# Performance work log

Measured on AMD Instinct MI355X. Metric: run time of the kernel, lower is better.

Reference implementation:

```python
import jax, jax.numpy as jnp
import numpy as np

N_HEADS = 16
DIM = 1024
BS, SLEN = 2, 2048
EPS = 1e-12  # F.normalize eps


def setup_inputs() -> dict:
    key = jax.random.key(0)
    ks = jax.random.split(key, 10)
    d = DIM
    inp = {
        "x": jax.random.normal(ks[0], (BS, SLEN, d), dtype=jnp.float32),
        # causal attention mask, as produced by get_masks(causal=True)
        "mask": jnp.tril(jnp.ones((SLEN, SLEN), dtype=bool))[None].repeat(BS, axis=0),
        "Wq": jax.random.normal(ks[1], (d, d), dtype=jnp.float32) / np.sqrt(d),
        "bq": jax.random.normal(ks[2], (d,), dtype=jnp.float32) * 0.02,
        "Wk": jax.random.normal(ks[3], (d, d), dtype=jnp.float32) / np.sqrt(d),
        "bk": jax.random.normal(ks[4], (d,), dtype=jnp.float32) * 0.02,
        "Wv": jax.random.normal(ks[5], (d, d), dtype=jnp.float32) / np.sqrt(d),
        "bv": jax.random.normal(ks[6], (d,), dtype=jnp.float32) * 0.02,
        "Wo": jax.random.normal(ks[7], (d, d), dtype=jnp.float32) / np.sqrt(d),
        "bo": jax.random.normal(ks[8], (d,), dtype=jnp.float32) * 0.02,
        # learnable scale for normalized (cosine) attention
        "attention_scale": jnp.ones((1,), dtype=jnp.float32) / np.sqrt(d // N_HEADS),
    }
    return inp


def _shape(t, bs, h, dph):
    # (bs, len, dim) -> (bs, h, len, dph)
    return t.reshape(bs, -1, h, dph).transpose(0, 2, 1, 3)


def reference(x, mask, Wq, bq, Wk, bk, Wv, bv, Wo, bo, attention_scale):
    bs, qlen, dim = x.shape
    h = N_HEADS
    dph = dim // h

    q = _shape(x @ Wq + bq, bs, h, dph)  # (bs, h, qlen, dph)
    k = _shape(x @ Wk + bk, bs, h, dph)
    v = _shape(x @ Wv + bv, bs, h, dph)

    # normalized (cosine) attention: L2-normalize q and k, learned scale
    q = q / jnp.maximum(jnp.linalg.norm(q, axis=-1, keepdims=True), EPS)
    k = k / jnp.maximum(jnp.linalg.norm(k, axis=-1, keepdims=True), EPS)
    q = q * attention_scale

    scores = jnp.einsum("bhqd,bhkd->bhqk", q, k)  # (bs, h, qlen, klen)
    scores = jnp.where(mask[:, None, :, :], scores, -jnp.inf)
    weights = jax.nn.softmax(scores, axis=-1)

    ctx = jnp.einsum("bhqk,bhkd->bhqd", weights, v)
    ctx = ctx.transpose(0, 2, 1, 3).reshape(bs, qlen, dim)
    return ctx @ Wo + bo
```

## Files before the change

kernel.cpp:

```cpp
#include <hip/hip_runtime.h>
#include <math.h>

#define NH 16
#define DPH 64
#define SLEN 2048
#define BSZ 2
#define DIM 1024
#define NTOK (BSZ * SLEN)
#define LOG2E 1.44269504088896f

typedef unsigned short ushortT;
typedef __attribute__((ext_vector_type(8))) short short8;
typedef __attribute__((ext_vector_type(4))) short s16x4;
typedef __attribute__((ext_vector_type(4))) float f32x4;

typedef __attribute__((address_space(1))) const unsigned int gu32c;
typedef __attribute__((address_space(3))) unsigned int lu32;

__device__ __forceinline__ void gld16(const void* g, void* l) {
    __builtin_amdgcn_global_load_lds((gu32c*)g, (lu32*)l, 16, 0, 0);
}

__device__ __forceinline__ ushortT f2bf(float f) {
    unsigned int u = __builtin_bit_cast(unsigned int, f);
    u = u + 0x7fffu + ((u >> 16) & 1u);
    return (ushortT)(u >> 16);
}

__global__ __launch_bounds__(256) void cvt_x(const float* __restrict__ x,
                                             ushortT* __restrict__ xb) {
    size_t i = (size_t)blockIdx.x * 256 + threadIdx.x;
    float4 a = *(const float4*)&x[i * 8];
    float4 b = *(const float4*)&x[i * 8 + 4];
    short8 v;
    v[0] = (short)f2bf(a.x); v[1] = (short)f2bf(a.y);
    v[2] = (short)f2bf(a.z); v[3] = (short)f2bf(a.w);
    v[4] = (short)f2bf(b.x); v[5] = (short)f2bf(b.y);
    v[6] = (short)f2bf(b.z); v[7] = (short)f2bf(b.w);
    *(short8*)&xb[i * 8] = v;
}

__global__ __launch_bounds__(256) void cvt_wt(const float* __restrict__ W0, const float* __restrict__ W1,
                                              const float* __restrict__ W2, const float* __restrict__ W3,
                                              ushortT* __restrict__ T0, ushortT* __restrict__ T1,
                                              ushortT* __restrict__ T2, ushortT* __restrict__ T3) {
    const float* W = blockIdx.z == 0 ? W0 : blockIdx.z == 1 ? W1 : blockIdx.z == 2 ? W2 : W3;
    ushortT* T = blockIdx.z == 0 ? T0 : blockIdx.z == 1 ? T1 : blockIdx.z == 2 ? T2 : T3;
    __shared__ float tile[64][65];
    const int tid = threadIdx.x;
    const int kb = blockIdx.y * 64, nb = blockIdx.x * 64;
#pragma unroll
    for (int it = 0; it < 4; it++) {
        int chunk = it * 256 + tid;
        int r = chunk >> 4, c4 = (chunk & 15) * 4;
        *(float4*)&tile[r][c4] = *(const float4*)&W[(size_t)(kb + r) * DIM + nb + c4];
    }
    __syncthreads();
#pragma unroll
    for (int it = 0; it < 2; it++) {
        int chunk = it * 256 + tid;
        int n = chunk >> 3, k8 = (chunk & 7) * 8;
        short8 o;
#pragma unroll
        for (int j = 0; j < 8; j++) o[j] = (short)f2bf(tile[k8 + j][n]);
        *(short8*)&T[(size_t)(nb + n) * DIM + kb + k8] = o;
    }
}

__global__ __launch_bounds__(512, 2) void gemm_qkv8(const ushortT* __restrict__ A,
                                                    const ushortT* __restrict__ Bt,
                                                    const float* __restrict__ bq,
                                                    const float* __restrict__ bk,
                                                    const float* __restrict__ bv,
                                                    const float* __restrict__ ascale,
                                                    ushortT* __restrict__ Qb,
                                                    ushortT* __restrict__ Kb,
                                                    ushortT* __restrict__ VF) {
    __shared__ __align__(16) ushortT lds[65536];
    const int tid = threadIdx.x;
    const int lane = tid & 63, wid = tid >> 6;
    const int wm = wid >> 2, wn = wid & 3;
    const int lo = lane & 15, hi = lane >> 4;
    const int bid = blockIdx.x;
    const int swz = (bid & 7) * 24 + (bid >> 3);
    const int bx = swz % 12, by = swz / 12;
    const int row0 = by * 256, col0 = bx * 256;
    const int srow2 = tid >> 2, sc = tid & 3;
    f32x4 acc[8][4] = {};
    short8 af[4], bfr[4];

    auto stage = [&](int isA, int buf, int ksh, int kt) {
        const ushortT* g = isA ? A : Bt;
        int r0 = isA ? row0 : col0;
        int base = (isA ? 0 : 32768) + (buf * 2 + ksh) * 8192;
#pragma unroll
        for (int r = 0; r < 2; r++) {
            int rl = r * 128 + srow2;
            int gch = sc ^ ((rl >> 1) & 3);
            gld16(&g[(size_t)(r0 + rl) * DIM + kt * 64 + ksh * 32 + gch * 8],
                  &lds[base + r * 4096 + tid * 8]);
        }
    };
    auto loadA = [&](int buf, int ks, int mh) {
        int base = (buf * 2 + ks) * 8192;
#pragma unroll
        for (int mm = 0; mm < 4; mm++) {
            int row = wm * 128 + (mh * 4 + mm) * 16 + lo;
            af[mm] = *(const short8*)&lds[base + row * 32 + (hi ^ ((row >> 1) & 3)) * 8];
        }
    };
    auto loadB = [&](int buf, int ks) {
        int base = 32768 + (buf * 2 + ks) * 8192;
#pragma unroll
        for (int n = 0; n < 4; n++) {
            int row = wn * 64 + n * 16 + lo;
            bfr[n] = *(const short8*)&lds[base + row * 32 + (hi ^ ((row >> 1) & 3)) * 8];
        }
    };
    auto mfma16 = [&](int mh) {
        __builtin_amdgcn_s_setprio(1);
#pragma unroll
        for (int mm = 0; mm < 4; mm++)
#pragma unroll
            for (int n = 0; n < 4; n++)
                acc[mh * 4 + mm][n] = __builtin_amdgcn_mfma_f32_16x16x32_bf16(
                    af[mm], bfr[n], acc[mh * 4 + mm][n], 0, 0, 0);
        __builtin_amdgcn_s_setprio(0);
    };

    stage(1, 0, 0, 0); stage(0, 0, 0, 0);
    stage(1, 0, 1, 0); stage(0, 0, 1, 0);
    stage(1, 1, 0, 1); stage(0, 1, 0, 1);

#pragma unroll 1
    for (int it = 0; it < 8; ++it) {
        const int o = it * 2 + 1;
        const bool more = (it < 7);
        asm volatile("s_waitcnt vmcnt(8)" ::: "memory");
        asm volatile("s_barrier" ::: "memory");
        loadA(0, 0, 0); loadB(0, 0);
        stage(1, 1, 1, o);
        mfma16(0);
        asm volatile("s_barrier" ::: "memory");
        loadA(0, 0, 1);
        stage(0, 1, 1, o);
        mfma16(1);
        asm volatile("s_waitcnt vmcnt(8)" ::: "memory");
        asm volatile("s_barrier" ::: "memory");
        loadA(0, 1, 0); loadB(0, 1);
        if (more) stage(1, 0, 0, o + 1);
        mfma16(0);
        asm volatile("s_barrier" ::: "memory");
        loadA(0, 1, 1);
        if (more) stage(0, 0, 0, o + 1);
        mfma16(1);
        if (more) { asm volatile("s_waitcnt vmcnt(8)" ::: "memory"); }
        else      { asm volatile("s_waitcnt vmcnt(4)" ::: "memory"); }
        asm volatile("s_barrier" ::: "memory");
        loadA(1, 0, 0); loadB(1, 0);
        if (more) stage(1, 0, 1, o + 1);
        mfma16(0);
        asm volatile("s_barrier" ::: "memory");
        loadA(1, 0, 1);
        if (more) stage(0, 0, 1, o + 1);
        mfma16(1);
        if (more) { asm volatile("s_waitcnt vmcnt(8)" ::: "memory"); }
        else      { asm volatile("s_waitcnt vmcnt(0)" ::: "memory"); }
        asm volatile("s_barrier" ::: "memory");
        loadA(1, 1, 0); loadB(1, 1);
        if (more) stage(1, 1, 0, o + 2);
        mfma16(0);
        asm volatile("s_barrier" ::: "memory");
        loadA(1, 1, 1);
        if (more) stage(0, 1, 0, o + 2);
        mfma16(1);
    }
    __syncthreads();

    const int cg = col0 + wn * 64;
    const int which = cg >> 10;
    const int cwin = cg & 1023;
    const int h = cwin >> 6;
    const int t0g = row0 + wm * 128;
    const int b = t0g >> 11, tok0 = t0g & (SLEN - 1);
    const float* bias = which == 0 ? bq : which == 1 ? bk : bv;

    float bb4[4];
#pragma unroll
    for (int n = 0; n < 4; n++) bb4[n] = bias[cwin + n * 16 + lo];
#pragma unroll
    for (int m = 0; m < 8; m++)
#pragma unroll
        for (int n = 0; n < 4; n++)
#pragma unroll
            for (int r = 0; r < 4; r++) acc[m][n][r] += bb4[n];

    if (which < 2) {
        float asc = (which == 0) ? ascale[0] * LOG2E : 1.0f;
#pragma unroll
        for (int m = 0; m < 8; m++)
#pragma unroll
            for (int r = 0; r < 4; r++) {
                float ss = acc[m][0][r] * acc[m][0][r] + acc[m][1][r] * acc[m][1][r] +
                           acc[m][2][r] * acc[m][2][r] + acc[m][3][r] * acc[m][3][r];
#pragma unroll
                for (int o = 8; o > 0; o >>= 1) ss += __shfl_xor(ss, o);
                float sc2 = asc / fmaxf(sqrtf(ss), 1e-12f);
#pragma unroll
                for (int n = 0; n < 4; n++) acc[m][n][r] *= sc2;
            }
    }

    ushortT* tl = &lds[wid * 8192];
    if (which < 2) {
#pragma unroll
        for (int m = 0; m < 8; m++)
#pragma unroll
            for (int n = 0; n < 4; n++)
#pragma unroll
                for (int r = 0; r < 4; r++) {
                    int row = m * 16 + 4 * hi + r;
                    int c = n * 2 + (lo >> 3);
                    tl[row * 64 + ((c ^ (row & 7)) << 3) + (lo & 7)] = f2bf(acc[m][n][r]);
                }
        ushortT* op = which == 0 ? Qb : Kb;
        const size_t base = ((size_t)(b * NH + h) * SLEN + tok0) * DPH;
#pragma unroll
        for (int j = 0; j < 16; j++) {
            int cid = j * 64 + lane;
            int rowL = cid >> 3, c = cid & 7;
            uint4 v = *(const uint4*)&tl[rowL * 64 + ((c ^ (rowL & 7)) << 3)];
            *(uint4*)&op[base + (size_t)cid * 8] = v;
        }
    } else {
#pragma unroll
        for (int m = 0; m < 8; m++)
#pragma unroll
            for (int n = 0; n < 4; n++)
#pragma unroll
                for (int r = 0; r < 4; r++) {
                    int row = m * 16 + 4 * hi + r;
                    int c = n * 2 + (lo >> 3);
                    tl[row * 64 + ((c ^ ((row >> 3) & 7)) << 3) + (lo & 7)] = f2bf(acc[m][n][r]);
                }
        const int bh = b * NH + h;
        const int kt0 = tok0 >> 6;
#pragma unroll
        for (int i = 0; i < 16; i++) {
            int kk = i >> 3;
            int c = i & 7;
            int jd = c >> 1, ks2 = c & 1;
            int colL = jd * 16 + lo;
            int c2 = colL >> 3;
            short8 v;
#pragma unroll
            for (int e = 0; e < 8; e++) {
                int rowL = kk * 64 + ks2 * 32 + 8 * hi + e;
                v[e] = (short)tl[rowL * 64 + ((c2 ^ ((rowL >> 3) & 7)) << 3) + (colL & 7)];
            }
            *(short8*)&VF[((size_t)bh * 32 + kt0 + kk) * 4096 + (size_t)(c * 64 + lane) * 8] = v;
        }
    }
}

__global__ __launch_bounds__(256) void gemm_oproj(const ushortT* __restrict__ A,
                                                  const ushortT* __restrict__ Bt,
                                                  const float* __restrict__ bias,
                                                  float* __restrict__ outF) {
    __shared__ __align__(16) unsigned char lbuf[32768];
    ushortT* As = (ushortT*)lbuf;
    ushortT* Bs = (ushortT*)(lbuf + 8192);
    const int tid = threadIdx.x;
    const int lane = tid & 63, wid = tid >> 6;
    const int wr = wid >> 1, wc = wid & 1;
    const int lo = lane & 15, hi = lane >> 4;
    const int row0 = blockIdx.y * 64, col0 = blockIdx.x * 128;
    const int r8 = lane >> 3, sp = lane & 7;
    const int srcoff = (sp ^ r8) << 3;
    f32x4 acc[2][4] = {};

    for (int kc = 0; kc < DIM; kc += 64) {
        __syncthreads();
#pragma unroll
        for (int it = 0; it < 2; it++) {
            int seg = it * 4 + wid;
            int row = seg * 8 + r8;
            gld16(&A[(size_t)(row0 + row) * DIM + kc + srcoff], &As[seg * 512]);
        }
#pragma unroll
        for (int it = 0; it < 4; it++) {
            int seg = it * 4 + wid;
            int row = seg * 8 + r8;
            gld16(&Bt[(size_t)(col0 + row) * DIM + kc + srcoff], &Bs[seg * 512]);
        }
        __syncthreads();
#pragma unroll
        for (int ks = 0; ks < 2; ks++) {
            short8 af[2], bfr[4];
#pragma unroll
            for (int m = 0; m < 2; m++) {
                int row = wr * 32 + m * 16 + lo;
                af[m] = *(const short8*)&As[row * 64 + (((ks * 4 + hi) ^ (row & 7)) << 3)];
            }
#pragma unroll
            for (int n = 0; n < 4; n++) {
                int row = wc * 64 + n * 16 + lo;
                bfr[n] = *(const short8*)&Bs[row * 64 + (((ks * 4 + hi) ^ (row & 7)) << 3)];
            }
#pragma unroll
            for (int m = 0; m < 2; m++)
#pragma unroll
                for (int n = 0; n < 4; n++)
                    acc[m][n] = __builtin_amdgcn_mfma_f32_16x16x32_bf16(af[m], bfr[n], acc[m][n], 0, 0, 0);
        }
    }

    float bb[4];
#pragma unroll
    for (int n = 0; n < 4; n++) bb[n] = bias[col0 + wc * 64 + n * 16 + lo];
#pragma unroll
    for (int m = 0; m < 2; m++)
#pragma unroll
        for (int n = 0; n < 4; n++)
#pragma unroll
            for (int r = 0; r < 4; r++) acc[m][n][r] += bb[n];

    __syncthreads();
    float* tl = (float*)(lbuf + wid * 8192);
#pragma unroll
    for (int m = 0; m < 2; m++)
#pragma unroll
        for (int n = 0; n < 4; n++)
#pragma unroll
            for (int r = 0; r < 4; r++) {
                int row = m * 16 + hi * 4 + r;
                int col = n * 16 + lo;
                int cc = col >> 2;
                tl[row * 64 + ((cc ^ (row & 7)) << 2) + (col & 3)] = acc[m][n][r];
            }
#pragma unroll
    for (int j = 0; j < 8; j++) {
        int cid = j * 64 + lane;
        int rowR = cid >> 4, cc = cid & 15;
        f32x4 v = *(const f32x4*)&tl[rowR * 64 + ((cc ^ (rowR & 7)) << 2)];
        int rg = row0 + wr * 32 + rowR;
        int cgl = col0 + wc * 64 + cc * 4;
        *(f32x4*)&outF[(size_t)rg * DIM + cgl] = v;
    }
}

__global__ __launch_bounds__(512, 4) void attn(const ushortT* __restrict__ Q,
                                               const ushortT* __restrict__ K,
                                               const ushortT* __restrict__ VF,
                                               const float* __restrict__ scale,
                                               ushortT* __restrict__ ctx) {
    __shared__ __align__(16) ushortT Ks[64 * 64];
    __shared__ __align__(16) ushortT Ps[8 * 16 * 64];
    const int tid = threadIdx.x, lane = tid & 63, wid = tid >> 6;
    const int wg = wid & 3, sg = wid >> 2;
    const int bh = blockIdx.x, p = blockIdx.y;
    const int qt = sg ? p : 31 - p;
    const int kbmax = 31 - p;
    const size_t hb = (size_t)bh * SLEN * DPH;
    const int lo = lane & 15, hi = lane >> 4;
    const float mshift = fabsf(scale[0]) * LOG2E;

    short8 aq[2];
    {
        const int qrow = qt * 64 + wg * 16 + lo;
#pragma unroll
        for (int ks = 0; ks < 2; ks++)
            aq[ks] = *(const short8*)&Q[hb + (size_t)qrow * DPH + ks * 32 + 8 * hi];
    }

    const int srow = tid >> 3, sslot = tid & 7;
    const int sldsoff = srow * 64 + ((sslot ^ (srow & 7)) << 3);
    uint4 kr = *(const uint4*)&K[hb + (size_t)srow * DPH + sslot * 8];
    *(uint4*)&Ks[sldsoff] = kr;
    __syncthreads();

    f32x4 accd[4] = {};
    float lp = 0.f;

    for (int kb = 0; kb <= kbmax; kb++) {
        if (kb < kbmax)
            kr = *(const uint4*)&K[hb + (size_t)((kb + 1) * 64 + srow) * DPH + sslot * 8];

        if (kb <= qt) {
            short8 bv[8];
            const ushortT* vt = &VF[(((size_t)bh * 32 + kb) * 512 + lane) * 8];
#pragma unroll
            for (int c = 0; c < 8; c++) bv[c] = *(const short8*)&vt[(size_t)c * 512];

            f32x4 sf[4] = {};
#pragma unroll
            for (int ks = 0; ks < 2; ks++)
#pragma unroll
                for (int j = 0; j < 4; j++) {
                    int row = j * 16 + lo;
                    short8 bk = *(const short8*)&Ks[row * 64 + (((ks * 4 + hi) ^ (row & 7)) << 3)];
                    sf[j] = __builtin_amdgcn_mfma_f32_16x16x32_bf16(bk, aq[ks], sf[j], 0, 0, 0);
                }

            if (kb == qt) {
#pragma unroll
                for (int j = 0; j < 4; j++)
#pragma unroll
                    for (int r = 0; r < 4; r++)
                        if (j * 16 + 4 * hi + r > wg * 16 + lo) sf[j][r] = -INFINITY;
            }

#pragma unroll
            for (int j = 0; j < 4; j++) {
                s16x4 pk;
#pragma unroll
                for (int r = 0; r < 4; r++) {
                    float pv = __builtin_amdgcn_exp2f(sf[j][r] - mshift);
                    lp += pv;
                    pk[r] = (short)f2bf(pv);
                }
                int slot = (4 * j + hi) ^ (2 * (lo & 7));
                *(s16x4*)&Ps[wid * 1024 + lo * 64 + slot * 4] = pk;
            }

#pragma unroll
            for (int ks = 0; ks < 2; ks++) {
                int slot0 = (8 * ks + 2 * hi) ^ (2 * (lo & 7));
                short8 ap = *(const short8*)&Ps[wid * 1024 + lo * 64 + slot0 * 4];
#pragma unroll
                for (int jd = 0; jd < 4; jd++)
                    accd[jd] = __builtin_amdgcn_mfma_f32_16x16x32_bf16(ap, bv[jd * 2 + ks], accd[jd], 0, 0, 0);
            }
        }

        __syncthreads();
        if (kb < kbmax) {
            *(uint4*)&Ks[sldsoff] = kr;
            __syncthreads();
        }
    }

    lp += __shfl_xor(lp, 16);
    lp += __shfl_xor(lp, 32);

    const int b = bh >> 4, h = bh & 15;
#pragma unroll
    for (int r = 0; r < 4; r++) {
        float lr = __shfl(lp, (lane & 48) | (4 * hi + r));
        float inv = 1.0f / lr;
        int t = qt * 64 + wg * 16 + 4 * hi + r;
#pragma unroll
        for (int jd = 0; jd < 4; jd++) {
            int d = jd * 16 + lo;
            ctx[(size_t)(b * SLEN + t) * DIM + h * 64 + d] = f2bf(accd[jd][r] * inv);
        }
    }
}

extern "C" void kernel_launch(void* const* d_in, const int* in_sizes, int n_in,
                              void* d_out, int out_size, void* d_ws,
                              size_t ws_size, hipStream_t stream) {
    const float* x = (const float*)d_in[0];
    const float* Wq = (const float*)d_in[2];
    const float* bq = (const float*)d_in[3];
    const float* Wk = (const float*)d_in[4];
    const float* bk = (const float*)d_in[5];
    const float* Wv = (const float*)d_in[6];
    const float* bv = (const float*)d_in[7];
    const float* Wo = (const float*)d_in[8];
    const float* bo = (const float*)d_in[9];
    const float* ascale = (const float*)d_in[10];
    float* outF = (float*)d_out;

    unsigned char* ws = (unsigned char*)d_ws;
    const size_t MB = 1u << 20;
    ushortT* xb = (ushortT*)(ws);
    ushortT* Wqkvt = (ushortT*)(ws + 8 * MB);
    ushortT* Wot = (ushortT*)(ws + 14 * MB);
    ushortT* Qb = (ushortT*)(ws + 16 * MB);
    ushortT* Kb = (ushortT*)(ws + 24 * MB);
    ushortT* VFb = (ushortT*)(ws + 32 * MB);
    ushortT* ctxb = (ushortT*)(ws + 40 * MB);

    cvt_x<<<NTOK * DIM / (8 * 256), 256, 0, stream>>>(x, xb);
    cvt_wt<<<dim3(16, 16, 4), 256, 0, stream>>>(Wq, Wk, Wv, Wo, Wqkvt,
                                                Wqkvt + (size_t)1024 * 1024,
                                                Wqkvt + (size_t)2048 * 1024, Wot);

    gemm_qkv8<<<dim3(192), 512, 0, stream>>>(xb, Wqkvt, bq, bk, bv, ascale, Qb, Kb, VFb);

    attn<<<dim3(32, 16), 512, 0, stream>>>(Qb, Kb, VFb, ascale, ctxb);

    gemm_oproj<<<dim3(DIM / 128, NTOK / 64), 256, 0, stream>>>(ctxb, Wot, bo, outF);
}
```

Before: 102.3 us.

## Merge conversion kernels, repipeline QKV GEMM, and rewrite O-proj as pipelined 128x128 GEMM

Merges the x and weight bf16 conversion kernels into one launch to save a kernel launch. Reorders the QKV GEMM's global-to-LDS staging so each k-half is staged as an A/B pair, with different waitcnt and barrier placement. Rewrites the output projection as a 128x128 tile GEMM with a 4-slot LDS ring buffer using direct global-to-LDS loads, raising per-wave MFMA work and overlapping loads with compute, plus a block swizzle. The extra barriers and larger tiles (fewer blocks, 256) may reduce occupancy.

```diff
diff --git a/kernel.cpp b/kernel.cpp
--- a/kernel.cpp
+++ b/kernel.cpp
@@ -27,28 +27,32 @@
     return (ushortT)(u >> 16);
 }
 
-__global__ __launch_bounds__(256) void cvt_x(const float* __restrict__ x,
-                                             ushortT* __restrict__ xb) {
-    size_t i = (size_t)blockIdx.x * 256 + threadIdx.x;
-    float4 a = *(const float4*)&x[i * 8];
-    float4 b = *(const float4*)&x[i * 8 + 4];
-    short8 v;
-    v[0] = (short)f2bf(a.x); v[1] = (short)f2bf(a.y);
-    v[2] = (short)f2bf(a.z); v[3] = (short)f2bf(a.w);
-    v[4] = (short)f2bf(b.x); v[5] = (short)f2bf(b.y);
-    v[6] = (short)f2bf(b.z); v[7] = (short)f2bf(b.w);
-    *(short8*)&xb[i * 8] = v;
-}
-
-__global__ __launch_bounds__(256) void cvt_wt(const float* __restrict__ W0, const float* __restrict__ W1,
-                                              const float* __restrict__ W2, const float* __restrict__ W3,
-                                              ushortT* __restrict__ T0, ushortT* __restrict__ T1,
-                                              ushortT* __restrict__ T2, ushortT* __restrict__ T3) {
-    const float* W = blockIdx.z == 0 ? W0 : blockIdx.z == 1 ? W1 : blockIdx.z == 2 ? W2 : W3;
-    ushortT* T = blockIdx.z == 0 ? T0 : blockIdx.z == 1 ? T1 : blockIdx.z == 2 ? T2 : T3;
+__global__ __launch_bounds__(256) void cvt_all(const float* __restrict__ x,
+                                               ushortT* __restrict__ xb,
+                                               const float* __restrict__ W0, const float* __restrict__ W1,
+                                               const float* __restrict__ W2, const float* __restrict__ W3,
+                                               ushortT* __restrict__ T0, ushortT* __restrict__ T1,
+                                               ushortT* __restrict__ T2, ushortT* __restrict__ T3) {
     __shared__ float tile[64][65];
     const int tid = threadIdx.x;
-    const int kb = blockIdx.y * 64, nb = blockIdx.x * 64;
+    const int bid = blockIdx.x;
+    if (bid < 2048) {
+        size_t i = (size_t)bid * 256 + tid;
+        float4 a = *(const float4*)&x[i * 8];
+        float4 b = *(const float4*)&x[i * 8 + 4];
+        short8 v;
+        v[0] = (short)f2bf(a.x); v[1] = (short)f2bf(a.y);
+        v[2] = (short)f2bf(a.z); v[3] = (short)f2bf(a.w);
+        v[4] = (short)f2bf(b.x); v[5] = (short)f2bf(b.y);
+        v[6] = (short)f2bf(b.z); v[7] = (short)f2bf(b.w);
+        *(short8*)&xb[i * 8] = v;
+        return;
+    }
+    const int widx = bid - 2048;
+    const int z = widx >> 8, rem = widx & 255;
+    const float* W = z == 0 ? W0 : z == 1 ? W1 : z == 2 ? W2 : W3;
+    ushortT* T = z == 0 ? T0 : z == 1 ? T1 : z == 2 ? T2 : T3;
+    const int kb = (rem >> 4) * 64, nb = (rem & 15) * 64;
 #pragma unroll
     for (int it = 0; it < 4; it++) {
         int chunk = it * 256 + tid;
@@ -128,52 +132,56 @@
         __builtin_amdgcn_s_setprio(0);
     };
 
-    stage(1, 0, 0, 0); stage(0, 0, 0, 0);
-    stage(1, 0, 1, 0); stage(0, 0, 1, 0);
-    stage(1, 1, 0, 1); stage(0, 1, 0, 1);
+    stage(0, 0, 0, 0); stage(1, 0, 0, 0);
+    stage(0, 0, 1, 0); stage(1, 0, 1, 0);
+    asm volatile("s_waitcnt vmcnt(4)" ::: "memory");
+    asm volatile("s_barrier" ::: "memory");
 
 #pragma unroll 1
     for (int it = 0; it < 8; ++it) {
-        const int o = it * 2 + 1;
+        const int e = it * 2, o = e + 1;
         const bool more = (it < 7);
-        asm volatile("s_waitcnt vmcnt(8)" ::: "memory");
-        asm volatile("s_barrier" ::: "memory");
         loadA(0, 0, 0); loadB(0, 0);
-        stage(1, 1, 1, o);
+        stage(0, 1, 0, o); stage(1, 1, 0, o);
+        asm volatile("s_barrier" ::: "memory");
         mfma16(0);
+        asm volatile("s_waitcnt vmcnt(4)" ::: "memory");
         asm volatile("s_barrier" ::: "memory");
         loadA(0, 0, 1);
-        stage(0, 1, 1, o);
+        asm volatile("s_barrier" ::: "memory");
         mfma16(1);
-        asm volatile("s_waitcnt vmcnt(8)" ::: "memory");
         asm volatile("s_barrier" ::: "memory");
         loadA(0, 1, 0); loadB(0, 1);
-        if (more) stage(1, 0, 0, o + 1);
+        stage(0, 1, 1, o); stage(1, 1, 1, o);
+        asm volatile("s_barrier" ::: "memory");
         mfma16(0);
+        asm volatile("s_waitcnt vmcnt(4)" ::: "memory");
         asm volatile("s_barrier" ::: "memory");
         loadA(0, 1, 1);
-        if (more) stage(0, 0, 0, o + 1);
+        asm volatile("s_barrier" ::: "memory");
         mfma16(1);
-        if (more) { asm volatile("s_waitcnt vmcnt(8)" ::: "memory"); }
-        else      { asm volatile("s_waitcnt vmcnt(4)" ::: "memory"); }
         asm volatile("s_barrier" ::: "memory");
         loadA(1, 0, 0); loadB(1, 0);
-        if (more) stage(1, 0, 1, o + 1);
+        if (more) { stage(0, 0, 0, e + 2); stage(1, 0, 0, e + 2); }
+        asm volatile("s_barrier" ::: "memory");
         mfma16(0);
+        if (more) { asm volatile("s_waitcnt vmcnt(4)" ::: "memory"); }
+        else      { asm volatile("s_waitcnt vmcnt(0)" ::: "memory"); }
         asm volatile("s_barrier" ::: "memory");
         loadA(1, 0, 1);
-        if (more) stage(0, 0, 1, o + 1);
+        asm volatile("s_barrier" ::: "memory");
         mfma16(1);
-        if (more) { asm volatile("s_waitcnt vmcnt(8)" ::: "memory"); }
-        else      { asm volatile("s_waitcnt vmcnt(0)" ::: "memory"); }
         asm volatile("s_barrier" ::: "memory");
         loadA(1, 1, 0); loadB(1, 1);
-        if (more) stage(1, 1, 0, o + 2);
+        if (more) { stage(0, 0, 1, e + 2); stage(1, 0, 1, e + 2); }
+        asm volatile("s_barrier" ::: "memory");
         mfma16(0);
+        if (more) { asm volatile("s_waitcnt vmcnt(4)" ::: "memory"); }
         asm volatile("s_barrier" ::: "memory");
         loadA(1, 1, 1);
-        if (more) stage(0, 1, 0, o + 2);
+        asm volatile("s_barrier" ::: "memory");
         mfma16(1);
+        asm volatile("s_barrier" ::: "memory");
     }
     __syncthreads();
 
@@ -254,9 +262,9 @@
             int c2 = colL >> 3;
             short8 v;
 #pragma unroll
-            for (int e = 0; e < 8; e++) {
-                int rowL = kk * 64 + ks2 * 32 + 8 * hi + e;
-                v[e] = (short)tl[rowL * 64 + ((c2 ^ ((rowL >> 3) & 7)) << 3) + (colL & 7)];
+            for (int e2 = 0; e2 < 8; e2++) {
+                int rowL = kk * 64 + ks2 * 32 + 8 * hi + e2;
+                v[e2] = (short)tl[rowL * 64 + ((c2 ^ ((rowL >> 3) & 7)) << 3) + (colL & 7)];
             }
             *(short8*)&VF[((size_t)bh * 32 + kt0 + kk) * 4096 + (size_t)(c * 64 + lane) * 8] = v;
         }
@@ -267,68 +275,108 @@
                                                   const ushortT* __restrict__ Bt,
                                                   const float* __restrict__ bias,
                                                   float* __restrict__ outF) {
-    __shared__ __align__(16) unsigned char lbuf[32768];
-    ushortT* As = (ushortT*)lbuf;
-    ushortT* Bs = (ushortT*)(lbuf + 8192);
+    __shared__ __align__(16) ushortT lds[32768];
     const int tid = threadIdx.x;
     const int lane = tid & 63, wid = tid >> 6;
     const int wr = wid >> 1, wc = wid & 1;
     const int lo = lane & 15, hi = lane >> 4;
-    const int row0 = blockIdx.y * 64, col0 = blockIdx.x * 128;
-    const int r8 = lane >> 3, sp = lane & 7;
-    const int srcoff = (sp ^ r8) << 3;
-    f32x4 acc[2][4] = {};
-
-    for (int kc = 0; kc < DIM; kc += 64) {
-        __syncthreads();
-#pragma unroll
-        for (int it = 0; it < 2; it++) {
-            int seg = it * 4 + wid;
-            int row = seg * 8 + r8;
-            gld16(&A[(size_t)(row0 + row) * DIM + kc + srcoff], &As[seg * 512]);
-        }
-#pragma unroll
-        for (int it = 0; it < 4; it++) {
-            int seg = it * 4 + wid;
-            int row = seg * 8 + r8;
-            gld16(&Bt[(size_t)(col0 + row) * DIM + kc + srcoff], &Bs[seg * 512]);
-        }
-        __syncthreads();
-#pragma unroll
-        for (int ks = 0; ks < 2; ks++) {
-            short8 af[2], bfr[4];
-#pragma unroll
-            for (int m = 0; m < 2; m++) {
-                int row = wr * 32 + m * 16 + lo;
-                af[m] = *(const short8*)&As[row * 64 + (((ks * 4 + hi) ^ (row & 7)) << 3)];
-            }
-#pragma unroll
-            for (int n = 0; n < 4; n++) {
-                int row = wc * 64 + n * 16 + lo;
-                bfr[n] = *(const short8*)&Bs[row * 64 + (((ks * 4 + hi) ^ (row & 7)) << 3)];
-            }
-#pragma unroll
-            for (int m = 0; m < 2; m++)
-#pragma unroll
-                for (int n = 0; n < 4; n++)
-                    acc[m][n] = __builtin_amdgcn_mfma_f32_16x16x32_bf16(af[m], bfr[n], acc[m][n], 0, 0, 0);
-        }
-    }
+    const int bid = blockIdx.x;
+    const int swz = (bid & 7) * 32 + (bid >> 3);
+    const int bx = swz & 7, by = swz >> 3;
+    const int row0 = by * 128, col0 = bx * 128;
+    f32x4 acc[4][4] = {};
+    short8 afO[4], bfO[4];
+
+    auto stageO = [&](int isA, int slot, int kh) {
+        const ushortT* g = isA ? A : Bt;
+        int r0 = isA ? row0 : col0;
+        int base = (isA ? 0 : 16384) + slot * 4096;
+#pragma unroll
+        for (int r = 0; r < 2; r++) {
+            int ch = r * 256 + tid;
+            int row = ch >> 2, kc = ch & 3;
+            gld16(&g[(size_t)(r0 + row) * DIM + kh * 32 + (kc ^ ((row >> 1) & 3)) * 8],
+                  &lds[base + r * 2048 + tid * 8]);
+        }
+    };
+    auto loadAO = [&](int slot) {
+        int base = slot * 4096;
+#pragma unroll
+        for (int m = 0; m < 4; m++) {
+            int row = wr * 64 + m * 16 + lo;
+            afO[m] = *(const short8*)&lds[base + row * 32 + (hi ^ ((row >> 1) & 3)) * 8];
+        }
+    };
+    auto loadBO = [&](int slot) {
+        int base = 16384 + slot * 4096;
+#pragma unroll
+        for (int n = 0; n < 4; n++) {
+            int row = wc * 64 + n * 16 + lo;
+            bfO[n] = *(const short8*)&lds[base + row * 32 + (hi ^ ((row >> 1) & 3)) * 8];
+        }
+    };
+    auto mfmaO = [&]() {
+        __builtin_amdgcn_s_setprio(1);
+#pragma unroll
+        for (int m = 0; m < 4; m++)
+#pragma unroll
+            for (int n = 0; n < 4; n++)
+                acc[m][n] = __builtin_amdgcn_mfma_f32_16x16x32_bf16(afO[m], bfO[n], acc[m][n], 0, 0, 0);
+        __builtin_amdgcn_s_setprio(0);
+    };
+
+    stageO(0, 0, 0); stageO(1, 0, 0);
+    stageO(0, 1, 1); stageO(1, 1, 1);
+    stageO(0, 2, 2); stageO(1, 2, 2);
+    asm volatile("s_waitcnt vmcnt(8)" ::: "memory");
+    asm volatile("s_barrier" ::: "memory");
+
+#pragma unroll 1
+    for (int it = 0; it < 8; ++it) {
+        const int k0 = it * 4;
+        const bool last = (it == 7);
+        loadAO(0); loadBO(0);
+        stageO(0, 3, k0 + 3); stageO(1, 3, k0 + 3);
+        asm volatile("s_barrier" ::: "memory");
+        mfmaO();
+        asm volatile("s_waitcnt vmcnt(8)" ::: "memory");
+        asm volatile("s_barrier" ::: "memory");
+        loadAO(1); loadBO(1);
+        if (!last) { stageO(0, 0, k0 + 4); stageO(1, 0, k0 + 4); }
+        asm volatile("s_barrier" ::: "memory");
+        mfmaO();
+        if (!last) { asm volatile("s_waitcnt vmcnt(8)" ::: "memory"); }
+        else       { asm volatile("s_waitcnt vmcnt(4)" ::: "memory"); }
+        asm volatile("s_barrier" ::: "memory");
+        loadAO(2); loadBO(2);
+        if (!last) { stageO(0, 1, k0 + 5); stageO(1, 1, k0 + 5); }
+        asm volatile("s_barrier" ::: "memory");
+        mfmaO();
+        if (!last) { asm volatile("s_waitcnt vmcnt(8)" ::: "memory"); }
+        else       { asm volatile("s_waitcnt vmcnt(0)" ::: "memory"); }
+        asm volatile("s_barrier" ::: "memory");
+        loadAO(3); loadBO(3);
+        if (!last) { stageO(0, 2, k0 + 6); stageO(1, 2, k0 + 6); }
+        asm volatile("s_barrier" ::: "memory");
+        mfmaO();
+        if (!last) { asm volatile("s_waitcnt vmcnt(8)" ::: "memory"); }
+        asm volatile("s_barrier" ::: "memory");
+    }
+    __syncthreads();
 
     float bb[4];
 #pragma unroll
     for (int n = 0; n < 4; n++) bb[n] = bias[col0 + wc * 64 + n * 16 + lo];
 #pragma unroll
-    for (int m = 0; m < 2; m++)
+    for (int m = 0; m < 4; m++)
 #pragma unroll
         for (int n = 0; n < 4; n++)
 #pragma unroll
             for (int r = 0; r < 4; r++) acc[m][n][r] += bb[n];
 
-    __syncthreads();
-    float* tl = (float*)(lbuf + wid * 8192);
-#pragma unroll
-    for (int m = 0; m < 2; m++)
+    float* tl = (float*)lds + wid * 4096;
+#pragma unroll
+    for (int m = 0; m < 4; m++)
 #pragma unroll
         for (int n = 0; n < 4; n++)
 #pragma unroll
@@ -339,11 +387,11 @@
                 tl[row * 64 + ((cc ^ (row & 7)) << 2) + (col & 3)] = acc[m][n][r];
             }
 #pragma unroll
-    for (int j = 0; j < 8; j++) {
+    for (int j = 0; j < 16; j++) {
         int cid = j * 64 + lane;
         int rowR = cid >> 4, cc = cid & 15;
         f32x4 v = *(const f32x4*)&tl[rowR * 64 + ((cc ^ (rowR & 7)) << 2)];
-        int rg = row0 + wr * 32 + rowR;
+        int rg = row0 + wr * 64 + rowR;
         int cgl = col0 + wc * 64 + cc * 4;
         *(f32x4*)&outF[(size_t)rg * DIM + cgl] = v;
     }
@@ -482,14 +530,13 @@
     ushortT* VFb = (ushortT*)(ws + 32 * MB);
     ushortT* ctxb = (ushortT*)(ws + 40 * MB);
 
-    cvt_x<<<NTOK * DIM / (8 * 256), 256, 0, stream>>>(x, xb);
-    cvt_wt<<<dim3(16, 16, 4), 256, 0, stream>>>(Wq, Wk, Wv, Wo, Wqkvt,
-                                                Wqkvt + (size_t)1024 * 1024,
-                                                Wqkvt + (size_t)2048 * 1024, Wot);
+    cvt_all<<<3072, 256, 0, stream>>>(x, xb, Wq, Wk, Wv, Wo, Wqkvt,
+                                      Wqkvt + (size_t)1024 * 1024,
+                                      Wqkvt + (size_t)2048 * 1024, Wot);
 
     gemm_qkv8<<<dim3(192), 512, 0, stream>>>(xb, Wqkvt, bq, bk, bv, ascale, Qb, Kb, VFb);
 
     attn<<<dim3(32, 16), 512, 0, stream>>>(Qb, Kb, VFb, ascale, ctxb);
 
-    gemm_oproj<<<dim3(DIM / 128, NTOK / 64), 256, 0, stream>>>(ctxb, Wot, bo, outF);
-}
+    gemm_oproj<<<dim3(256), 256, 0, stream>>>(ctxb, Wot, bo, outF);
+}
```

Result: slower. 106.4 us (+4.0%).
